# Optimization experiments

Measured on AMD Instinct MI355X. Metric: run time of the kernel, lower is better.

Reference implementation:

```python
import jax, jax.numpy as jnp
import numpy as np


def setup_inputs() -> dict:
    key = jax.random.key(0)
    ks = jax.random.split(key, 8)
    N, C, T, V = 32, 64, 256, 25
    OUT, INTER, S = 64, 16, 3
    W_SCALE = 0.05  # keep complex softmax exp() well-conditioned
    return {
        "x_real": jax.random.normal(ks[0], (N, C, T, V), jnp.float32),
        "x_imag": jax.random.normal(ks[1], (N, C, T, V), jnp.float32),
        "A": jax.random.uniform(ks[2], (S, V, V), jnp.float32),
        "PA": jax.random.normal(ks[3], (S, V, V), jnp.float32) * 1e-3,
        "Wa": jax.random.normal(ks[4], (S, 2 * INTER, 2 * C), jnp.float32) * W_SCALE,
        "ba": jnp.zeros((S, 2 * INTER), jnp.float32),
        "Wb": jax.random.normal(ks[5], (S, 2 * INTER, 2 * C), jnp.float32) * W_SCALE,
        "bb": jnp.zeros((S, 2 * INTER), jnp.float32),
        "Wd": jax.random.normal(ks[6], (S, 2 * OUT, 2 * C), jnp.float32) * W_SCALE,
        "bd": jnp.zeros((S, 2 * OUT), jnp.float32),
        "bn_weight": jnp.ones((OUT,), jnp.float32),
        "bn_bias": jnp.zeros((OUT,), jnp.float32),
    }


def _cconv1x1(z, W, b):
    # C_Conv2d with k=1: 1x1 conv over concat(real, imag) channels.
    zc = jnp.concatenate([z.real, z.imag], axis=1)          # [N, 2*Cin, T, V]
    o = jnp.einsum("oc,nctv->notv", W, zc) + b[None, :, None, None]
    h = W.shape[0] // 2
    return jax.lax.complex(o[:, :h], o[:, h:])              # [N, Cout, T, V] complex


def _forward(x_real, x_imag, A, PA, Wa, ba, Wb, bb, Wd, bd, bn_weight, bn_bias):
    x = jax.lax.complex(x_real, x_imag)                     # [N, C, T, V]
    N, C, T, V = x.shape
    inter = Wa.shape[1] // 2
    Afull = A + PA                                          # [3, V, V] real
    X2 = x.reshape(N, C * T, V)
    y = None
    for i in range(A.shape[0]):
        A1 = _cconv1x1(x, Wa[i], ba[i])                     # [N, inter, T, V]
        A1 = A1.transpose(0, 3, 1, 2).reshape(N, V, inter * T)
        A2 = _cconv1x1(x, Wb[i], bb[i]).reshape(N, inter * T, V)
        S = jnp.matmul(A1, A2) / (inter * T)                # [N, V, V] complex
        # complex softmax over dim=1 (no max-subtraction, faithful to C_softmax)
        ez = jnp.exp(S)
        S = ez / jnp.sum(ez, axis=1, keepdims=True)
        S = S + Afull[i]
        z = jnp.matmul(X2, S).reshape(N, C, T, V)
        z = _cconv1x1(z, Wd[i], bd[i])                      # [N, OUT, T, V]
        y = z if y is None else y + z
    # C_BatchNorm2d on complex input: complex mean, real variance = E|y-mu|^2
    mu = jnp.mean(y, axis=(0, 2, 3))                        # [OUT] complex
    var = jnp.mean(jnp.abs(y - mu[None, :, None, None]) ** 2, axis=(0, 2, 3))
    yn = (y - mu[None, :, None, None]) / jnp.sqrt(var + 1e-5)[None, :, None, None]
    yn = yn * bn_weight[None, :, None, None] + bn_bias[None, :, None, None]
    yn = yn + x  # down = identity (in_channels == out_channels)
    return jnp.stack([yn.real, yn.imag])                    # [2, N, OUT, T, V] real


def reference(x_real, x_imag, A, PA, Wa, ba, Wb, bb, Wd, bd, bn_weight, bn_bias):
    return _forward(x_real, x_imag, A, PA, Wa, ba, Wb, bb, Wd, bd, bn_weight, bn_bias)
```

## Files before the change

kernel.cpp:

```cpp
#include <hip/hip_runtime.h>
#include <hip/hip_bf16.h>
#include <stdint.h>

#define NN 32
#define CC 64
#define TTOT 256
#define VV 25
#define NS 3
constexpr int TV  = TTOT * VV;
constexpr int CTV = CC * TV;
constexpr size_t PLANE = (size_t)NN * CTV;

typedef unsigned short ushort_t;
using short8 = __attribute__((ext_vector_type(8))) short;
using f32x4  = __attribute__((ext_vector_type(4))) float;

static __device__ __forceinline__ ushort_t f2bf(float f) {
  __hip_bfloat16 h = __float2bfloat16(f);
  return reinterpret_cast<ushort_t&>(h);
}
static __device__ __forceinline__ float bf2f(ushort_t h) {
  union { uint32_t u; float f; } v; v.u = ((uint32_t)h) << 16;
  return v.f;
}
static __device__ __forceinline__ int SWZ(int row, int k) {
  return ((row << 7) + k) ^ ((row & 7) << 3);
}
static __device__ __forceinline__ f32x4 mfma16(short8 a, short8 b, f32x4 c) {
  return __builtin_amdgcn_mfma_f32_16x16x32_bf16(a, b, c, 0, 0, 0);
}

__global__ __launch_bounds__(256) void k0_wfrag(
    const float* __restrict__ Wd, const float* __restrict__ Wa,
    const float* __restrict__ Wb, ushort_t* __restrict__ wfrag,
    ushort_t* __restrict__ wab)
{
  const int i = blockIdx.x;
  for (int e = threadIdx.x; e < 16384; e += 256) {
    int mt = e >> 11, ks = (e >> 9) & 3, l = (e >> 3) & 63, j = e & 7;
    int r  = mt * 16 + (l & 15);
    int kp = ks * 32 + ((l >> 4) << 3) + j;
    int c = kp >> 1, comp = kp & 1;
    wfrag[(size_t)i * 16384 + e] = f2bf(Wd[(size_t)i * 16384 + r * 128 + comp * 64 + c]);
  }
  for (int e = threadIdx.x; e < 8192; e += 256) {
    int mt = e >> 11, ks = (e >> 9) & 3, l = (e >> 3) & 63, j = e & 7;
    int r  = mt * 16 + (l & 15);
    int kp = ks * 32 + ((l >> 4) << 3) + j;
    float v = (r < 32) ? Wa[((size_t)i * 32 + r) * 128 + kp]
                       : Wb[((size_t)i * 32 + (r - 32)) * 128 + kp];
    wab[(size_t)i * 8192 + e] = f2bf(v);
  }
}

__global__ __launch_bounds__(256) void k1_spart(
    const float* __restrict__ xr, const float* __restrict__ xi,
    const ushort_t* __restrict__ wab, const float* __restrict__ ba,
    const float* __restrict__ bb, float* __restrict__ Spart)
{
  const int tc = blockIdx.x, n = blockIdx.y;
  const int tid = threadIdx.x, lane = tid & 63, wv = tid >> 6;
  const int r16 = lane & 15, gw = lane >> 4;
  __shared__ alignas(16) ushort_t zc[128 * 128];
  __shared__ alignas(16) ushort_t Ga[32 * 128];
  __shared__ alignas(16) ushort_t Gb[32 * 128];

  for (int e4 = tid; e4 < 128 * 25; e4 += 256) {
    int c = e4 / 25, q = e4 % 25;
    const float* src = (c < 64) ? xr : xi;
    float4 w = *(const float4*)&src[(size_t)n * CTV + (c & 63) * TV + tc * 100 + q * 4];
#pragma unroll
    for (int jj = 0; jj < 4; ++jj) {
      int g = q * 4 + jj, t = g / 25, v = g - t * 25;
      zc[SWZ(t * 32 + v, c)] = f2bf(((const float*)&w)[jj]);
    }
  }
  for (int e = tid; e < 28 * 128; e += 256) {
    int r7 = e >> 7, c = e & 127;
    int t = r7 / 7, vv = 25 + r7 % 7;
    zc[SWZ(t * 32 + vv, c)] = 0;
  }

  const int mu = wv >> 1, nv = wv & 1;

  for (int i = 0; i < NS; ++i) {
    __syncthreads();

    {
      short8 afr[4];
#pragma unroll
      for (int ks = 0; ks < 4; ++ks)
        afr[ks] = *(const short8*)&wab[((((size_t)i * 4 + wv) * 4 + ks) * 64 + lane) * 8];
      float bias[4];
#pragma unroll
      for (int j = 0; j < 4; ++j) {
        int row = wv * 16 + gw * 4 + j;
        bias[j] = (row < 32) ? ba[i * 32 + row] : bb[i * 32 + (row - 32)];
      }
      ushort_t* gbuf = (wv < 2) ? Ga : Gb;
      const int half = (wv & 1) * 64;
      for (int nt = 0; nt < 8; ++nt) {
        f32x4 acc = {0.f, 0.f, 0.f, 0.f};
        const int brow = nt * 16 + r16;
#pragma unroll
        for (int ks = 0; ks < 4; ++ks) {
          short8 bfr = *(const short8*)&zc[SWZ(brow, ks * 32 + gw * 8)];
          acc = mfma16(afr[ks], bfr, acc);
        }
        int pos2 = nt * 16 + r16;
        int t = pos2 >> 5, v = pos2 & 31;
        int k0w = half + t * 16 + gw * 4;
        uint32_t w0 = (uint32_t)f2bf(acc[0] + bias[0]) | ((uint32_t)f2bf(acc[1] + bias[1]) << 16);
        uint32_t w1 = (uint32_t)f2bf(acc[2] + bias[2]) | ((uint32_t)f2bf(acc[3] + bias[3]) << 16);
        uint2 pk; pk.x = w0; pk.y = w1;
        *(uint2*)&gbuf[SWZ(v, k0w)] = pk;
      }
    }
    __syncthreads();

    {
      const int urow = mu * 16 + r16;
      const int vrow = nv * 16 + r16;
      f32x4 Prr = {0.f,0.f,0.f,0.f}, Pii = {0.f,0.f,0.f,0.f};
      f32x4 Pri = {0.f,0.f,0.f,0.f}, Pir = {0.f,0.f,0.f,0.f};
#pragma unroll
      for (int ks = 0; ks < 2; ++ks) {
        int ko = ks * 32 + gw * 8;
        short8 arF = *(const short8*)&Ga[SWZ(urow, ko)];
        short8 aiF = *(const short8*)&Ga[SWZ(urow, 64 + ko)];
        short8 brF = *(const short8*)&Gb[SWZ(vrow, ko)];
        short8 biF = *(const short8*)&Gb[SWZ(vrow, 64 + ko)];
        Prr = mfma16(arF, brF, Prr);
        Pii = mfma16(aiF, biF, Pii);
        Pri = mfma16(arF, biF, Pri);
        Pir = mfma16(aiF, brF, Pir);
      }
#pragma unroll
      for (int j = 0; j < 4; ++j) {
        int u = mu * 16 + gw * 4 + j;
        int v = nv * 16 + r16;
        if (u < VV && v < VV) {
          size_t idx = ((((size_t)i * NN + n) * 64 + tc) * 625 + u * 25 + v) * 2;
          Spart[idx]     = Prr[j] - Pii[j];
          Spart[idx + 1] = Pri[j] + Pir[j];
        }
      }
    }
  }
}

__global__ __launch_bounds__(256) void k2_softmax(
    const float* __restrict__ Spart, const float* __restrict__ Aw,
    const float* __restrict__ PA, ushort_t* __restrict__ sfrag)
{
  const int i = blockIdx.x, n = blockIdx.y, tid = threadIdx.x;
  __shared__ float ez[625 * 2];
  __shared__ float den[25 * 2];
  for (int e = tid; e < 625; e += 256) {
    float sr = 0.f, si = 0.f;
    const float* p = Spart + (((size_t)i * NN + n) * 64 * 625 + e) * 2;
    for (int tcb = 0; tcb < 64; ++tcb) { sr += p[0]; si += p[1]; p += 625 * 2; }
    sr *= (1.f / 4096.f); si *= (1.f / 4096.f);
    float m = expf(sr);
    ez[e * 2] = m * cosf(si);
    ez[e * 2 + 1] = m * sinf(si);
  }
  __syncthreads();
  if (tid < 25) {
    float dr = 0.f, di = 0.f;
    for (int u = 0; u < 25; ++u) { dr += ez[(u * 25 + tid) * 2]; di += ez[(u * 25 + tid) * 2 + 1]; }
    float inv = 1.f / (dr * dr + di * di);
    den[tid * 2] = dr * inv; den[tid * 2 + 1] = -di * inv;
  }
  __syncthreads();
  for (int e = tid; e < 625; e += 256) {
    int v = e % 25;
    float er = ez[e * 2], ei = ez[e * 2 + 1];
    float dr = den[v * 2], di = den[v * 2 + 1];
    float outr = er * dr - ei * di + Aw[i * 625 + e] + PA[i * 625 + e];
    float outi = er * di + ei * dr;
    ez[e * 2] = outr; ez[e * 2 + 1] = outi;
  }
  __syncthreads();
  for (int e = tid; e < 768; e += 256) {
    int l = e & 63, nt = (e >> 6) & 1, m = e >> 7;
    int u0 = (l >> 4) << 3, v = nt * 16 + (l & 15);
    short8 pk;
#pragma unroll
    for (int j = 0; j < 8; ++j) {
      int u = u0 + j;
      float val = 0.f;
      if (u < VV && v < VV) {
        float sr_ = ez[(u * 25 + v) * 2], si_ = ez[(u * 25 + v) * 2 + 1];
        float base = (m < 2) ? sr_ : (m < 4) ? si_ : -si_;
        if (m & 1) { float hi = bf2f(f2bf(base)); val = base - hi; }
        else val = base;
      }
      pk[j] = (short)f2bf(val);
    }
    *(short8*)&sfrag[((size_t)(i * NN + n) * 768 + e) * 8] = pk;
  }
}

__global__ __launch_bounds__(512) void k3_y(
    const float* __restrict__ xr, const float* __restrict__ xi,
    const ushort_t* __restrict__ sfrag, const ushort_t* __restrict__ wfrag,
    const float* __restrict__ bd, float* __restrict__ out,
    float* __restrict__ bnpart)
{
  const int tcc = blockIdx.x, n = blockIdx.y;
  const int tid = threadIdx.x, lane = tid & 63, wv = tid >> 6;
  const int tp = wv >> 2, mq = wv & 3;
  const int r16 = lane & 15, gw = lane >> 4;
  __shared__ alignas(16) ushort_t zbuf[2][64 * 128];
  __shared__ float stats[2][128][2];

  short8 xf[2][2];
#pragma unroll
  for (int mtl = 0; mtl < 2; ++mtl) {
    int mt = mq * 2 + mtl;
    int mrow = mt * 16 + r16;
    int c = mrow & 63, t01 = mrow >> 6;
    int t = tcc * 4 + tp * 2 + t01;
#pragma unroll
    for (int comp = 0; comp < 2; ++comp) {
      const float* p = (comp ? xi : xr) + (size_t)n * CTV + c * TV + t * VV;
      short8 f;
#pragma unroll
      for (int j = 0; j < 8; ++j) {
        int u = gw * 8 + j;
        f[j] = (u < VV) ? (short)f2bf(p[u]) : (short)0;
      }
      xf[mtl][comp] = f;
    }
  }

  f32x4 acc[2][4];
#pragma unroll
  for (int a = 0; a < 2; ++a)
#pragma unroll
    for (int b = 0; b < 4; ++b) acc[a][b] = {0.f, 0.f, 0.f, 0.f};

#pragma unroll 1
  for (int i = 0; i < NS; ++i) {
    const ushort_t* sb = sfrag + (size_t)(i * NN + n) * 6144;
    short8 bfrag[6][2];
#pragma unroll
    for (int m = 0; m < 6; ++m)
#pragma unroll
      for (int nt = 0; nt < 2; ++nt)
        bfrag[m][nt] = *(const short8*)&sb[((m * 2 + nt) * 64 + lane) * 8];

    __syncthreads();

#pragma unroll
    for (int mtl = 0; mtl < 2; ++mtl) {
      const int mt = mq * 2 + mtl;
      const int t01 = mt >> 2;
      const int cbase = (mt & 3) * 16 + gw * 4;
      short8 Ar = xf[mtl][0], Ai = xf[mtl][1];
#pragma unroll
      for (int nt = 0; nt < 2; ++nt) {
        f32x4 zr = {0.f, 0.f, 0.f, 0.f}, zi = {0.f, 0.f, 0.f, 0.f};
        zr = mfma16(Ar, bfrag[0][nt], zr);
        zr = mfma16(Ar, bfrag[1][nt], zr);
        zr = mfma16(Ai, bfrag[4][nt], zr);
        zr = mfma16(Ai, bfrag[5][nt], zr);
        zi = mfma16(Ar, bfrag[2][nt], zi);
        zi = mfma16(Ar, bfrag[3][nt], zi);
        zi = mfma16(Ai, bfrag[0][nt], zi);
        zi = mfma16(Ai, bfrag[1][nt], zi);
        int pos2 = t01 * 32 + nt * 16 + r16;
        short8 pk;
#pragma unroll
        for (int j = 0; j < 4; ++j) {
          pk[2 * j]     = (short)f2bf(zr[j]);
          pk[2 * j + 1] = (short)f2bf(zi[j]);
        }
        *(short8*)&zbuf[tp][SWZ(pos2, cbase * 2)] = pk;
      }
    }
    __syncthreads();

    const ushort_t* wb = wfrag + (size_t)i * 16384;
#pragma unroll
    for (int ks = 0; ks < 4; ++ks) {
      short8 af0 = *(const short8*)&wb[(((mq * 2 + 0) * 4 + ks) * 64 + lane) * 8];
      short8 af1 = *(const short8*)&wb[(((mq * 2 + 1) * 4 + ks) * 64 + lane) * 8];
#pragma unroll
      for (int nt = 0; nt < 4; ++nt) {
        int brow = nt * 16 + r16;
        short8 bf = *(const short8*)&zbuf[tp][SWZ(brow, ks * 32 + gw * 8)];
        acc[0][nt] = mfma16(af0, bf, acc[0][nt]);
        acc[1][nt] = mfma16(af1, bf, acc[1][nt]);
      }
    }
  }

#pragma unroll
  for (int mtl = 0; mtl < 2; ++mtl) {
#pragma unroll
    for (int j = 0; j < 4; ++j) {
      int row = (mq * 2 + mtl) * 16 + gw * 4 + j;
      float bias = bd[row] + bd[128 + row] + bd[256 + row];
      float s = 0.f, q = 0.f;
#pragma unroll
      for (int nt = 0; nt < 4; ++nt) {
        int pos2 = nt * 16 + r16;
        int t01 = pos2 >> 5, v = pos2 & 31;
        float val = acc[mtl][nt][j] + bias;
        if (v < VV) {
          int ri = row >> 6, o = row & 63;
          int t = tcc * 4 + tp * 2 + t01;
          out[(size_t)ri * PLANE + (size_t)n * CTV + o * TV + t * VV + v] = val;
          s += val; q += val * val;
        }
      }
#pragma unroll
      for (int d = 1; d < 16; d <<= 1) { s += __shfl_xor(s, d); q += __shfl_xor(q, d); }
      if (r16 == 0) { stats[tp][row][0] = s; stats[tp][row][1] = q; }
    }
  }
  __syncthreads();
  if (tid < 128) {
    size_t b = (size_t)(n * 64 + tcc);
    bnpart[(b * 128 + tid) * 2]     = stats[0][tid][0] + stats[1][tid][0];
    bnpart[(b * 128 + tid) * 2 + 1] = stats[0][tid][1] + stats[1][tid][1];
  }
}

__global__ __launch_bounds__(256) void k4_stats(
    const float* __restrict__ bnpart, const float* __restrict__ bnw,
    const float* __restrict__ bnb, float* __restrict__ coeff)
{
  const int o = blockIdx.x, tid = threadIdx.x;
  float sr = 0.f, qr = 0.f, si = 0.f, qi = 0.f;
  for (int b = tid; b < 2048; b += 256) {
    const float* p = bnpart + ((size_t)b * 128 + o) * 2;
    sr += p[0]; qr += p[1];
    const float* p2 = bnpart + ((size_t)b * 128 + 64 + o) * 2;
    si += p2[0]; qi += p2[1];
  }
#pragma unroll
  for (int d = 1; d < 64; d <<= 1) {
    sr += __shfl_xor(sr, d); qr += __shfl_xor(qr, d);
    si += __shfl_xor(si, d); qi += __shfl_xor(qi, d);
  }
  __shared__ float red[4][4];
  int lane = tid & 63, wv = tid >> 6;
  if (lane == 0) { red[wv][0] = sr; red[wv][1] = qr; red[wv][2] = si; red[wv][3] = qi; }
  __syncthreads();
  if (tid == 0) {
    sr = red[0][0] + red[1][0] + red[2][0] + red[3][0];
    qr = red[0][1] + red[1][1] + red[2][1] + red[3][1];
    si = red[0][2] + red[1][2] + red[2][2] + red[3][2];
    qi = red[0][3] + red[1][3] + red[2][3] + red[3][3];
    const float invM = 1.f / (float)((size_t)NN * TTOT * VV);
    float mur = sr * invM, mui = si * invM;
    float var = (qr + qi) * invM - mur * mur - mui * mui;
    float inv = rsqrtf(var + 1e-5f);
    coeff[o * 4 + 0] = mur; coeff[o * 4 + 1] = mui;
    coeff[o * 4 + 2] = inv * bnw[o]; coeff[o * 4 + 3] = bnb[o];
  }
}

__global__ __launch_bounds__(256) void k5_norm(
    const float* __restrict__ xr, const float* __restrict__ xi,
    const float* __restrict__ coeff, float* __restrict__ out)
{
  size_t idx0 = ((size_t)blockIdx.x * 256 + threadIdx.x) * 4;
  size_t stride = (size_t)gridDim.x * 256 * 4;
  for (size_t e = idx0; e < PLANE; e += stride) {
    int o = (int)((e / TV) & 63);
    float4 cf = *(const float4*)&coeff[o * 4];
    float4 yr = *(float4*)&out[e];
    float4 yi = *(float4*)&out[PLANE + e];
    float4 vr = *(const float4*)&xr[e];
    float4 vi = *(const float4*)&xi[e];
    yr.x = (yr.x - cf.x) * cf.z + cf.w + vr.x;
    yr.y = (yr.y - cf.x) * cf.z + cf.w + vr.y;
    yr.z = (yr.z - cf.x) * cf.z + cf.w + vr.z;
    yr.w = (yr.w - cf.x) * cf.z + cf.w + vr.w;
    yi.x = (yi.x - cf.y) * cf.z + vi.x;
    yi.y = (yi.y - cf.y) * cf.z + vi.y;
    yi.z = (yi.z - cf.y) * cf.z + vi.z;
    yi.w = (yi.w - cf.y) * cf.z + vi.w;
    *(float4*)&out[e] = yr;
    *(float4*)&out[PLANE + e] = yi;
  }
}

extern "C" void kernel_launch(void* const* d_in, const int* in_sizes, int n_in,
                              void* d_out, int out_size, void* d_ws, size_t ws_size,
                              hipStream_t stream) {
  const float* xr  = (const float*)d_in[0];
  const float* xi  = (const float*)d_in[1];
  const float* Aw  = (const float*)d_in[2];
  const float* PA  = (const float*)d_in[3];
  const float* Wa  = (const float*)d_in[4];
  const float* ba  = (const float*)d_in[5];
  const float* Wb  = (const float*)d_in[6];
  const float* bb  = (const float*)d_in[7];
  const float* Wd  = (const float*)d_in[8];
  const float* bd  = (const float*)d_in[9];
  const float* bnw = (const float*)d_in[10];
  const float* bnb = (const float*)d_in[11];
  float* out = (float*)d_out;
  float* ws = (float*)d_ws;

  float*    Spart  = ws;
  float*    bnpart = ws;
  ushort_t* sfrag  = (ushort_t*)(ws + 7680000);
  ushort_t* wfrag  = (ushort_t*)(ws + 7974912);
  ushort_t* wab    = (ushort_t*)(ws + 7999488);
  float*    coeff  = ws + 8011776;

  k0_wfrag<<<NS, 256, 0, stream>>>(Wd, Wa, Wb, wfrag, wab);
  k1_spart<<<dim3(64, NN), 256, 0, stream>>>(xr, xi, wab, ba, bb, Spart);
  k2_softmax<<<dim3(NS, NN), 256, 0, stream>>>(Spart, Aw, PA, sfrag);
  k3_y<<<dim3(64, NN), 512, 0, stream>>>(xr, xi, sfrag, wfrag, bd, out, bnpart);
  k4_stats<<<64, 256, 0, stream>>>(bnpart, bnw, bnb, coeff);
  k5_norm<<<6400, 256, 0, stream>>>(xr, xi, coeff, out);
}
```

Measured before the change: 265.0 us.

## Restructure k3 to one timestep per block with all subsets staged first

The fused graph-mix plus Wd-projection kernel now handles one timestep per 256-thread block instead of four per 512-thread block. It computes the z fragments for all three subsets into separate LDS buffers with a single barrier, where the old code synchronised twice per subset. Sign-negated S fragments are derived in-register from loaded ones, so only four of the six fragment groups are read. The trade-off is four times as many blocks and BN partial records, and k4 is extended to reduce over the larger partial array.

New measurement: 291.5 us. 1.1x slower.

```diff
diff --git a/kernel.cpp b/kernel.cpp
--- a/kernel.cpp
+++ b/kernel.cpp
@@ -28,6 +28,12 @@
 }
 static __device__ __forceinline__ f32x4 mfma16(short8 a, short8 b, f32x4 c) {
   return __builtin_amdgcn_mfma_f32_16x16x32_bf16(a, b, c, 0, 0, 0);
+}
+static __device__ __forceinline__ short8 negbf8(short8 x) {
+  short8 r;
+#pragma unroll
+  for (int j = 0; j < 8; ++j) r[j] = x[j] ^ (short)0x8000;
+  return r;
 }
 
 __global__ __launch_bounds__(256) void k0_wfrag(
@@ -202,130 +208,111 @@
   }
 }
 
-__global__ __launch_bounds__(512) void k3_y(
+__global__ __launch_bounds__(256, 6) void k3_y(
     const float* __restrict__ xr, const float* __restrict__ xi,
     const ushort_t* __restrict__ sfrag, const ushort_t* __restrict__ wfrag,
     const float* __restrict__ bd, float* __restrict__ out,
     float* __restrict__ bnpart)
 {
-  const int tcc = blockIdx.x, n = blockIdx.y;
+  const int t = blockIdx.x, n = blockIdx.y;
   const int tid = threadIdx.x, lane = tid & 63, wv = tid >> 6;
-  const int tp = wv >> 2, mq = wv & 3;
   const int r16 = lane & 15, gw = lane >> 4;
-  __shared__ alignas(16) ushort_t zbuf[2][64 * 128];
-  __shared__ float stats[2][128][2];
-
-  short8 xf[2][2];
-#pragma unroll
-  for (int mtl = 0; mtl < 2; ++mtl) {
-    int mt = mq * 2 + mtl;
-    int mrow = mt * 16 + r16;
-    int c = mrow & 63, t01 = mrow >> 6;
-    int t = tcc * 4 + tp * 2 + t01;
-#pragma unroll
-    for (int comp = 0; comp < 2; ++comp) {
-      const float* p = (comp ? xi : xr) + (size_t)n * CTV + c * TV + t * VV;
-      short8 f;
-#pragma unroll
-      for (int j = 0; j < 8; ++j) {
-        int u = gw * 8 + j;
-        f[j] = (u < VV) ? (short)f2bf(p[u]) : (short)0;
-      }
-      xf[mtl][comp] = f;
-    }
-  }
-
-  f32x4 acc[2][4];
-#pragma unroll
-  for (int a = 0; a < 2; ++a)
-#pragma unroll
-    for (int b = 0; b < 4; ++b) acc[a][b] = {0.f, 0.f, 0.f, 0.f};
+  __shared__ alignas(16) ushort_t zbuf[3][32 * 128];
+  __shared__ float stats[128][2];
+
+  short8 xfr, xfi;
+  {
+    const size_t base = (size_t)n * CTV + (size_t)(wv * 16 + r16) * TV + (size_t)t * VV;
+    const float* pr = xr + base;
+    const float* pi_ = xi + base;
+#pragma unroll
+    for (int j = 0; j < 8; ++j) {
+      int u = gw * 8 + j;
+      xfr[j] = (u < VV) ? (short)f2bf(pr[u]) : (short)0;
+      xfi[j] = (u < VV) ? (short)f2bf(pi_[u]) : (short)0;
+    }
+  }
 
 #pragma unroll 1
   for (int i = 0; i < NS; ++i) {
     const ushort_t* sb = sfrag + (size_t)(i * NN + n) * 6144;
-    short8 bfrag[6][2];
-#pragma unroll
-    for (int m = 0; m < 6; ++m)
+    short8 bf[4][2];
+#pragma unroll
+    for (int m = 0; m < 4; ++m)
 #pragma unroll
       for (int nt = 0; nt < 2; ++nt)
-        bfrag[m][nt] = *(const short8*)&sb[((m * 2 + nt) * 64 + lane) * 8];
-
-    __syncthreads();
-
-#pragma unroll
-    for (int mtl = 0; mtl < 2; ++mtl) {
-      const int mt = mq * 2 + mtl;
-      const int t01 = mt >> 2;
-      const int cbase = (mt & 3) * 16 + gw * 4;
-      short8 Ar = xf[mtl][0], Ai = xf[mtl][1];
-#pragma unroll
-      for (int nt = 0; nt < 2; ++nt) {
-        f32x4 zr = {0.f, 0.f, 0.f, 0.f}, zi = {0.f, 0.f, 0.f, 0.f};
-        zr = mfma16(Ar, bfrag[0][nt], zr);
-        zr = mfma16(Ar, bfrag[1][nt], zr);
-        zr = mfma16(Ai, bfrag[4][nt], zr);
-        zr = mfma16(Ai, bfrag[5][nt], zr);
-        zi = mfma16(Ar, bfrag[2][nt], zi);
-        zi = mfma16(Ar, bfrag[3][nt], zi);
-        zi = mfma16(Ai, bfrag[0][nt], zi);
-        zi = mfma16(Ai, bfrag[1][nt], zi);
-        int pos2 = t01 * 32 + nt * 16 + r16;
-        short8 pk;
-#pragma unroll
-        for (int j = 0; j < 4; ++j) {
-          pk[2 * j]     = (short)f2bf(zr[j]);
-          pk[2 * j + 1] = (short)f2bf(zi[j]);
-        }
-        *(short8*)&zbuf[tp][SWZ(pos2, cbase * 2)] = pk;
-      }
-    }
-    __syncthreads();
-
+        bf[m][nt] = *(const short8*)&sb[((m * 2 + nt) * 64 + lane) * 8];
+#pragma unroll
+    for (int nt = 0; nt < 2; ++nt) {
+      short8 ms0 = negbf8(bf[2][nt]), ms1 = negbf8(bf[3][nt]);
+      f32x4 zr = {0.f, 0.f, 0.f, 0.f}, zi = {0.f, 0.f, 0.f, 0.f};
+      zr = mfma16(xfr, bf[0][nt], zr);
+      zr = mfma16(xfr, bf[1][nt], zr);
+      zr = mfma16(xfi, ms0, zr);
+      zr = mfma16(xfi, ms1, zr);
+      zi = mfma16(xfr, bf[2][nt], zi);
+      zi = mfma16(xfr, bf[3][nt], zi);
+      zi = mfma16(xfi, bf[0][nt], zi);
+      zi = mfma16(xfi, bf[1][nt], zi);
+      short8 pk;
+#pragma unroll
+      for (int j = 0; j < 4; ++j) {
+        pk[2 * j]     = (short)f2bf(zr[j]);
+        pk[2 * j + 1] = (short)f2bf(zi[j]);
+      }
+      *(short8*)&zbuf[i][SWZ(nt * 16 + r16, wv * 32 + gw * 8)] = pk;
+    }
+  }
+  __syncthreads();
+
+  f32x4 acc[2][2];
+#pragma unroll
+  for (int a = 0; a < 2; ++a)
+#pragma unroll
+    for (int b = 0; b < 2; ++b) acc[a][b] = {0.f, 0.f, 0.f, 0.f};
+
+#pragma unroll 1
+  for (int i = 0; i < NS; ++i) {
     const ushort_t* wb = wfrag + (size_t)i * 16384;
 #pragma unroll
-    for (int ks = 0; ks < 4; ++ks) {
-      short8 af0 = *(const short8*)&wb[(((mq * 2 + 0) * 4 + ks) * 64 + lane) * 8];
-      short8 af1 = *(const short8*)&wb[(((mq * 2 + 1) * 4 + ks) * 64 + lane) * 8];
-#pragma unroll
-      for (int nt = 0; nt < 4; ++nt) {
-        int brow = nt * 16 + r16;
-        short8 bf = *(const short8*)&zbuf[tp][SWZ(brow, ks * 32 + gw * 8)];
-        acc[0][nt] = mfma16(af0, bf, acc[0][nt]);
-        acc[1][nt] = mfma16(af1, bf, acc[1][nt]);
-      }
-    }
-  }
-
-#pragma unroll
-  for (int mtl = 0; mtl < 2; ++mtl) {
+    for (int m = 0; m < 4; ++m) {
+      short8 bf0 = *(const short8*)&zbuf[i][SWZ(r16, m * 32 + gw * 8)];
+      short8 bf1 = *(const short8*)&zbuf[i][SWZ(16 + r16, m * 32 + gw * 8)];
+      short8 a0 = *(const short8*)&wb[(((wv * 2 + 0) * 4 + m) * 64 + lane) * 8];
+      short8 a1 = *(const short8*)&wb[(((wv * 2 + 1) * 4 + m) * 64 + lane) * 8];
+      acc[0][0] = mfma16(a0, bf0, acc[0][0]);
+      acc[0][1] = mfma16(a0, bf1, acc[0][1]);
+      acc[1][0] = mfma16(a1, bf0, acc[1][0]);
+      acc[1][1] = mfma16(a1, bf1, acc[1][1]);
+    }
+  }
+
+#pragma unroll
+  for (int otl = 0; otl < 2; ++otl) {
 #pragma unroll
     for (int j = 0; j < 4; ++j) {
-      int row = (mq * 2 + mtl) * 16 + gw * 4 + j;
+      int row = (wv * 2 + otl) * 16 + gw * 4 + j;
       float bias = bd[row] + bd[128 + row] + bd[256 + row];
       float s = 0.f, q = 0.f;
 #pragma unroll
-      for (int nt = 0; nt < 4; ++nt) {
-        int pos2 = nt * 16 + r16;
-        int t01 = pos2 >> 5, v = pos2 & 31;
-        float val = acc[mtl][nt][j] + bias;
+      for (int nt = 0; nt < 2; ++nt) {
+        int v = nt * 16 + r16;
+        float val = acc[otl][nt][j] + bias;
         if (v < VV) {
-          int ri = row >> 6, o = row & 63;
-          int t = tcc * 4 + tp * 2 + t01;
-          out[(size_t)ri * PLANE + (size_t)n * CTV + o * TV + t * VV + v] = val;
+          out[(size_t)(row >> 6) * PLANE + (size_t)n * CTV + (row & 63) * TV + t * VV + v] = val;
           s += val; q += val * val;
         }
       }
 #pragma unroll
       for (int d = 1; d < 16; d <<= 1) { s += __shfl_xor(s, d); q += __shfl_xor(q, d); }
-      if (r16 == 0) { stats[tp][row][0] = s; stats[tp][row][1] = q; }
+      if (r16 == 0) { stats[row][0] = s; stats[row][1] = q; }
     }
   }
   __syncthreads();
   if (tid < 128) {
-    size_t b = (size_t)(n * 64 + tcc);
-    bnpart[(b * 128 + tid) * 2]     = stats[0][tid][0] + stats[1][tid][0];
-    bnpart[(b * 128 + tid) * 2 + 1] = stats[0][tid][1] + stats[1][tid][1];
+    size_t b = (size_t)n * 256 + t;
+    bnpart[(b * 128 + tid) * 2]     = stats[tid][0];
+    bnpart[(b * 128 + tid) * 2 + 1] = stats[tid][1];
   }
 }
 
@@ -335,7 +322,7 @@
 {
   const int o = blockIdx.x, tid = threadIdx.x;
   float sr = 0.f, qr = 0.f, si = 0.f, qi = 0.f;
-  for (int b = tid; b < 2048; b += 256) {
+  for (int b = tid; b < 8192; b += 256) {
     const float* p = bnpart + ((size_t)b * 128 + o) * 2;
     sr += p[0]; qr += p[1];
     const float* p2 = bnpart + ((size_t)b * 128 + 64 + o) * 2;
@@ -418,7 +405,7 @@
   k0_wfrag<<<NS, 256, 0, stream>>>(Wd, Wa, Wb, wfrag, wab);
   k1_spart<<<dim3(64, NN), 256, 0, stream>>>(xr, xi, wab, ba, bb, Spart);
   k2_softmax<<<dim3(NS, NN), 256, 0, stream>>>(Spart, Aw, PA, sfrag);
-  k3_y<<<dim3(64, NN), 512, 0, stream>>>(xr, xi, sfrag, wfrag, bd, out, bnpart);
+  k3_y<<<dim3(TTOT, NN), 256, 0, stream>>>(xr, xi, sfrag, wfrag, bd, out, bnpart);
   k4_stats<<<64, 256, 0, stream>>>(bnpart, bnw, bnb, coeff);
   k5_norm<<<6400, 256, 0, stream>>>(xr, xi, coeff, out);
 }
```
